# Performance work log

Measured on AMD Instinct MI355X. Metric: run time of the kernel, lower is better.

## Reference

```python
import jax, jax.numpy as jnp
import numpy as np

EMB_DIM = 768
NUM_HEADS = 12
OUT_DIM = 768


def setup_inputs() -> dict:
    key = jax.random.key(0)
    k_x, k_q, k_k, k_v, k_o = jax.random.split(key, 5)
    B, N, D = 8, 1024, EMB_DIM
    s = 1.0 / np.sqrt(D)
    return {
        "x": jax.random.normal(k_x, (B, N, D), dtype=jnp.float32),
        # torch nn.Linear weights are stored [out_features, in_features]
        "Wq": jax.random.normal(k_q, (D, D), dtype=jnp.float32) * s,
        "Wk": jax.random.normal(k_k, (D, D), dtype=jnp.float32) * s,
        "Wv": jax.random.normal(k_v, (D, D), dtype=jnp.float32) * s,
        "Wo": jax.random.normal(k_o, (OUT_DIM, D), dtype=jnp.float32) * s,
    }


def _split_heads(t, H):
    # [B, N, D] -> [B*H, N, D//H]  (heads folded into batch, per einsum 'b i d')
    B, N, D = t.shape
    return t.reshape(B, N, H, D // H).transpose(0, 2, 1, 3).reshape(B * H, N, D // H)


def _merge_heads(t, B, H):
    BH, N, dh = t.shape
    return t.reshape(B, H, N, dh).transpose(0, 2, 1, 3).reshape(B, N, H * dh)


def reference(x, Wq, Wk, Wv, Wo):
    B, N, D = x.shape
    H = NUM_HEADS
    dh = D // H
    # q/k/v projections (torch Linear: y = x @ W.T, no bias)
    q = _split_heads(x @ Wq.T, H)
    k = _split_heads(x @ Wk.T, H)
    v = _split_heads(x @ Wv.T, H)
    scale = dh ** (-0.5)
    # dots: 'b i d , b j d -> b i j' -> full [B*H, N, N] score matrix
    dots = jnp.einsum('bid,bjd->bij', q, k) * scale
    attn = jax.nn.softmax(dots, axis=-1)
    # dropout p=0.0 -> identity
    # vect: 'b i d , b d j -> b i j' == attn @ v
    vect = jnp.einsum('bij,bjd->bid', attn, v)
    out = _merge_heads(vect, B, H) @ Wo.T
    return out
```

## Files before the change

kernel.cpp:

```cpp
#include <hip/hip_runtime.h>
#include <hip/hip_bf16.h>
#include <stdint.h>


typedef __bf16 bf16x8 __attribute__((ext_vector_type(8)));
typedef __bf16 bf16x4 __attribute__((ext_vector_type(4)));
typedef float f32x4 __attribute__((ext_vector_type(4)));

#define GAS __attribute__((address_space(1)))
#define LAS __attribute__((address_space(3)))

__device__ __forceinline__ void glds16(const short* gp, short* lp) {
  __builtin_amdgcn_global_load_lds((const GAS void*)gp, (LAS void*)lp, 16, 0, 0);
}

__device__ __forceinline__ float fast_exp2(float x) {
#if __has_builtin(__builtin_amdgcn_exp2f)
  return __builtin_amdgcn_exp2f(x);
#else
  return __expf(x * 0.6931471805599453f);
#endif
}

__device__ __forceinline__ short bfbits(float f) {
  __bf16 b = (__bf16)f;
  union { __bf16 b; short s; } cv; cv.b = b;
  return cv.s;
}

__device__ __forceinline__ void stage8_f32(const float* __restrict__ src, short* dst) {
  float4 f0 = ((const float4*)src)[0];
  float4 f1 = ((const float4*)src)[1];
  bf16x8 t;
  t[0] = (__bf16)f0.x; t[1] = (__bf16)f0.y; t[2] = (__bf16)f0.z; t[3] = (__bf16)f0.w;
  t[4] = (__bf16)f1.x; t[5] = (__bf16)f1.y; t[6] = (__bf16)f1.z; t[7] = (__bf16)f1.w;
  *(bf16x8*)dst = t;
}

__global__ __launch_bounds__(256) void convert_kernel(
    const float* __restrict__ x, const float* __restrict__ Wq,
    const float* __restrict__ Wk, const float* __restrict__ Wv,
    const float* __restrict__ Wo,
    short* __restrict__ xb, short* __restrict__ wqkv, short* __restrict__ wob) {
  int u0 = blockIdx.x * 1024 + threadIdx.x;
#pragma unroll
  for (int i = 0; i < 4; ++i) {
    int u = u0 + i * 256;
    const float* src; short* dst;
    if (u < 786432) { src = x + (size_t)u * 8; dst = xb + (size_t)u * 8; }
    else if (u < 1007616) {
      int r = u - 786432;
      int wsel = r / 73728, off = r % 73728;
      const float* W = (wsel == 0) ? Wq : (wsel == 1) ? Wk : Wv;
      src = W + (size_t)off * 8;
      dst = wqkv + (size_t)r * 8;
    } else {
      int r = u - 1007616;
      src = Wo + (size_t)r * 8; dst = wob + (size_t)r * 8;
    }
    stage8_f32(src, dst);
  }
}

__device__ __forceinline__ void stage_half(const short* __restrict__ g, short* l,
                                           int w, int lane) {
#pragma unroll
  for (int p = 0; p < 2; ++p) {
    int c = (w * 2 + p) * 64 + lane;
    int row = c >> 3;
    int cs = ((c & 7) ^ (row & 7)) * 8;
    glds16(g + (size_t)row * 768 + cs, l + c * 8);
  }
}

__device__ __forceinline__ void bar_fence() {
  asm volatile("" ::: "memory");
  __builtin_amdgcn_s_barrier();
  asm volatile("" ::: "memory");
}

__device__ __forceinline__ void load_a8(const short* base, int wr, int l16, int quad,
                                        bf16x8 (&fa)[4][2]) {
#pragma unroll
  for (int mf = 0; mf < 4; ++mf)
#pragma unroll
    for (int kk = 0; kk < 2; ++kk) {
      int row = wr * 64 + mf * 16 + l16;
      fa[mf][kk] = *(const bf16x8*)&base[row * 64 + ((((kk << 2) + quad) ^ (row & 7)) << 3)];
    }
}

__device__ __forceinline__ void load_b4(const short* base, int rbase, int l16, int quad,
                                        bf16x8 (&fb)[2][2]) {
#pragma unroll
  for (int nf = 0; nf < 2; ++nf)
#pragma unroll
    for (int kk = 0; kk < 2; ++kk) {
      int row = rbase + nf * 16 + l16;
      fb[nf][kk] = *(const bf16x8*)&base[row * 64 + ((((kk << 2) + quad) ^ (row & 7)) << 3)];
    }
}

__device__ __forceinline__ void mma16(const bf16x8 (&fa)[4][2], const bf16x8 (&fb)[2][2],
                                      f32x4 (&acc)[4][4], int nf0) {
  __builtin_amdgcn_s_setprio(1);
#pragma unroll
  for (int kk = 0; kk < 2; ++kk)
#pragma unroll
    for (int mf = 0; mf < 4; ++mf)
#pragma unroll
      for (int nf = 0; nf < 2; ++nf)
        acc[mf][nf0 + nf] = __builtin_amdgcn_mfma_f32_16x16x32_bf16(
            fa[mf][kk], fb[nf][kk], acc[mf][nf0 + nf], 0, 0, 0);
  __builtin_amdgcn_s_setprio(0);
}

__global__ __launch_bounds__(512, 2) void gemm_qkv(
    const short* __restrict__ xb, const short* __restrict__ wqkv,
    short* __restrict__ q, short* __restrict__ k, short* __restrict__ vt) {
  const int lin = blockIdx.x;
  const int swz = (lin & 7) * 36 + (lin >> 3);
  const int bx = swz & 31;
  const int by = swz >> 5;
  const int m0 = bx * 256;
  const int n0g = by * 256;
  const int tid = threadIdx.x;
  const int w = tid >> 6, lane = tid & 63, l16 = lane & 15, quad = lane >> 4;
  const int wr = w >> 2, wc = w & 3;

  __shared__ short lds[2][2][2][8192];

  const short* Asrc = xb + (size_t)m0 * 768;
  const short* Bsrc = wqkv + (size_t)n0g * 768;

  f32x4 acc[2][4][4];
#pragma unroll
  for (int h = 0; h < 2; ++h)
#pragma unroll
    for (int i = 0; i < 4; ++i)
#pragma unroll
      for (int j = 0; j < 4; ++j) acc[h][i][j] = (f32x4){0.f, 0.f, 0.f, 0.f};

  stage_half(Asrc, &lds[0][0][0][0], w, lane);
  stage_half(Bsrc, &lds[0][1][0][0], w, lane);
  stage_half(Bsrc + 98304, &lds[0][1][1][0], w, lane);
  stage_half(Asrc + 98304, &lds[0][0][1][0], w, lane);
  stage_half(Asrc + 64, &lds[1][0][0][0], w, lane);
  stage_half(Bsrc + 64, &lds[1][1][0][0], w, lane);
  stage_half(Bsrc + 98304 + 64, &lds[1][1][1][0], w, lane);
  asm volatile("s_waitcnt vmcnt(6)" ::: "memory");
  bar_fence();

  const int bh = wc >> 1;
  const int rb0 = (wc & 1) * 64;
  const short* bb0 = &lds[0][1][bh][0];
  const short* bb1 = &lds[1][1][bh][0];

  bf16x8 fa[4][2], fb0[2][2], fb1[2][2];

  for (int i = 0; i < 6; ++i) {
    const int t1 = 2 * i + 1, t2 = 2 * i + 2, t3 = 2 * i + 3;
    const bool pf = (i < 5);

    load_a8(&lds[0][0][0][0], wr, l16, quad, fa);
    load_b4(bb0, rb0, l16, quad, fb0);
    stage_half(Asrc + 98304 + (size_t)t1 * 64, &lds[1][0][1][0], w, lane);
    bar_fence();
    mma16(fa, fb0, acc[0], 0);
    bar_fence();
    load_b4(bb0, rb0 + 32, l16, quad, fb1);
    if (pf) stage_half(Asrc + (size_t)t2 * 64, &lds[0][0][0][0], w, lane);
    bar_fence();
    mma16(fa, fb1, acc[0], 2);
    bar_fence();
    load_a8(&lds[0][0][1][0], wr, l16, quad, fa);
    if (pf) stage_half(Bsrc + (size_t)t2 * 64, &lds[0][1][0][0], w, lane);
    bar_fence();
    mma16(fa, fb1, acc[1], 2);
    bar_fence();
    if (pf) {
      stage_half(Bsrc + 98304 + (size_t)t2 * 64, &lds[0][1][1][0], w, lane);
      asm volatile("s_waitcnt vmcnt(6)" ::: "memory");
    } else {
      asm volatile("s_waitcnt vmcnt(0)" ::: "memory");
    }
    bar_fence();
    mma16(fa, fb0, acc[1], 0);
    bar_fence();

    load_a8(&lds[1][0][0][0], wr, l16, quad, fa);
    load_b4(bb1, rb0, l16, quad, fb0);
    if (pf) stage_half(Asrc + 98304 + (size_t)t2 * 64, &lds[0][0][1][0], w, lane);
    bar_fence();
    mma16(fa, fb0, acc[0], 0);
    bar_fence();
    load_b4(bb1, rb0 + 32, l16, quad, fb1);
    if (pf) stage_half(Asrc + (size_t)t3 * 64, &lds[1][0][0][0], w, lane);
    bar_fence();
    mma16(fa, fb1, acc[0], 2);
    bar_fence();
    load_a8(&lds[1][0][1][0], wr, l16, quad, fa);
    if (pf) stage_half(Bsrc + (size_t)t3 * 64, &lds[1][1][0][0], w, lane);
    bar_fence();
    mma16(fa, fb1, acc[1], 2);
    bar_fence();
    if (pf) stage_half(Bsrc + 98304 + (size_t)t3 * 64, &lds[1][1][1][0], w, lane);
    asm volatile("s_waitcnt vmcnt(6)" ::: "memory");
    bar_fence();
    mma16(fa, fb0, acc[1], 0);
    bar_fence();
  }

  const int wsel = by / 3;
  const int nl0 = (by % 3) * 256 + wc * 64;
  if (wsel == 2) {
#pragma unroll
    for (int h = 0; h < 2; ++h)
#pragma unroll
      for (int mf = 0; mf < 4; ++mf)
#pragma unroll
        for (int nf = 0; nf < 4; ++nf) {
          int token = m0 + h * 128 + wr * 64 + mf * 16 + quad * 4;
          int nl = nl0 + nf * 16 + l16;
          int bhh = (token >> 10) * 12 + (nl >> 6);
          short tmp[4];
#pragma unroll
          for (int r = 0; r < 4; ++r) tmp[r] = bfbits(acc[h][mf][nf][r]);
          *(uint2*)(vt + (size_t)bhh * 65536 + (size_t)(nl & 63) * 1024 + (token & 1023)) =
              *(const uint2*)tmp;
        }
  } else {
    short* C = wsel ? k : q;
    const float sc = wsel ? 1.0f : 0.1803368801111244f;
#pragma unroll
    for (int h = 0; h < 2; ++h)
#pragma unroll
      for (int mf = 0; mf < 4; ++mf)
#pragma unroll
        for (int nf = 0; nf < 4; ++nf)
#pragma unroll
          for (int r = 0; r < 4; ++r) {
            int row = m0 + h * 128 + wr * 64 + mf * 16 + quad * 4 + r;
            int nl = nl0 + nf * 16 + l16;
            C[(size_t)row * 768 + nl] = bfbits(acc[h][mf][nf][r] * sc);
          }
  }
}

__global__ __launch_bounds__(256) void attn_kernel(
    const short* __restrict__ q, const short* __restrict__ k,
    const short* __restrict__ vt, short* __restrict__ vect) {
  const int bh = blockIdx.x % 96;
  const int qt = blockIdx.x / 96;
  const int b = bh / 12, h = bh % 12;
  const int m0 = qt * 64;
  const int tid = threadIdx.x;
  const int w = tid >> 6, lane = tid & 63, l16 = lane & 15, quad = lane >> 4;

  __shared__ short sK[128 * 64];
  __shared__ short sVt[64 * 128];

  const size_t base = (size_t)b * 786432 + (size_t)h * 64;
  const size_t vbase = (size_t)bh * 65536;

#pragma unroll
  for (int p = 0; p < 2; ++p) {
    int lin = (w * 2 + p) * 64 + lane;
    int row = lin >> 3;
    int cs = ((lin & 7) ^ (row & 7)) * 8;
    glds16(q + base + (size_t)(m0 + row) * 768 + cs, &sK[lin * 8]);
  }
  __syncthreads();
  bf16x8 bq[2];
#pragma unroll
  for (int kk = 0; kk < 2; ++kk) {
    int row = w * 16 + l16;
    bq[kk] = *(const bf16x8*)&sK[row * 64 + (((kk * 4 + quad) ^ (row & 7)) << 3)];
  }

  f32x4 l4 = (f32x4){0.f, 0.f, 0.f, 0.f};
  f32x4 oacc[4];
#pragma unroll
  for (int td = 0; td < 4; ++td) oacc[td] = (f32x4){0.f, 0.f, 0.f, 0.f};

  for (int j0 = 0; j0 < 1024; j0 += 128) {
    __syncthreads();
#pragma unroll
    for (int p = 0; p < 4; ++p) {
      int lin = (w * 4 + p) * 64 + lane;
      int row = lin >> 3;
      int cs = ((lin & 7) ^ (row & 7)) * 8;
      glds16(k + base + (size_t)(j0 + row) * 768 + cs, &sK[lin * 8]);
    }
#pragma unroll
    for (int p = 0; p < 4; ++p) {
      int lin = (w * 4 + p) * 64 + lane;
      int row = lin >> 4;
      int c = lin & 15;
      int cs = (c ^ (row & 15)) * 8;
      glds16(vt + vbase + (size_t)row * 1024 + j0 + cs, &sVt[lin * 8]);
    }
    __syncthreads();

#pragma unroll
    for (int jh = 0; jh < 2; ++jh) {
      f32x4 s[4];
#pragma unroll
      for (int ti = 0; ti < 4; ++ti) s[ti] = (f32x4){0.f, 0.f, 0.f, 0.f};
#pragma unroll
      for (int kk = 0; kk < 2; ++kk)
#pragma unroll
        for (int ti = 0; ti < 4; ++ti) {
          int row = jh * 64 + ti * 16 + l16;
          bf16x8 a = *(const bf16x8*)&sK[row * 64 + (((kk * 4 + quad) ^ (row & 7)) << 3)];
          s[ti] = __builtin_amdgcn_mfma_f32_16x16x32_bf16(a, bq[kk], s[ti], 0, 0, 0);
        }

      bf16x4 pb[4];
#pragma unroll
      for (int ti = 0; ti < 4; ++ti) {
        f32x4 e;
        e[0] = fast_exp2(s[ti][0]);
        e[1] = fast_exp2(s[ti][1]);
        e[2] = fast_exp2(s[ti][2]);
        e[3] = fast_exp2(s[ti][3]);
        l4 += e;
        bf16x4 tb;
        tb[0] = (__bf16)e[0]; tb[1] = (__bf16)e[1];
        tb[2] = (__bf16)e[2]; tb[3] = (__bf16)e[3];
        pb[ti] = tb;
      }

#pragma unroll
      for (int t2 = 0; t2 < 2; ++t2) {
        union { bf16x4 hh[2]; bf16x8 v; } bp;
        bp.hh[0] = pb[2 * t2];
        bp.hh[1] = pb[2 * t2 + 1];
#pragma unroll
        for (int td = 0; td < 4; ++td) {
          int row = td * 16 + l16;
          int o1 = jh * 64 + t2 * 32 + quad * 4;
          int c1 = o1 >> 3, w1 = o1 & 7;
          int c2 = c1 + 2;
          union { uint2 u[2]; bf16x8 v; } tmp;
          tmp.u[0] = *(const uint2*)&sVt[row * 128 + ((c1 ^ (row & 15)) << 3) + w1];
          tmp.u[1] = *(const uint2*)&sVt[row * 128 + ((c2 ^ (row & 15)) << 3) + w1];
          oacc[td] = __builtin_amdgcn_mfma_f32_16x16x32_bf16(tmp.v, bp.v, oacc[td], 0, 0, 0);
        }
      }
    }
  }

  float l = (l4[0] + l4[1]) + (l4[2] + l4[3]);
  l += __shfl_xor(l, 16);
  l += __shfl_xor(l, 32);
  float inv = 1.0f / l;
  int i_tok = m0 + w * 16 + l16;
#pragma unroll
  for (int td = 0; td < 4; ++td) {
    short tmp[4];
#pragma unroll
    for (int r = 0; r < 4; ++r) tmp[r] = bfbits(oacc[td][r] * inv);
    *(uint2*)(vect + base + (size_t)i_tok * 768 + td * 16 + quad * 4) = *(const uint2*)tmp;
  }
}

__global__ __launch_bounds__(256) void gemm_out(
    const short* __restrict__ vect, const short* __restrict__ wob,
    float* __restrict__ out) {
  const int m0 = blockIdx.x * 64;
  const int n0 = blockIdx.y * 128;
  const int tid = threadIdx.x;
  const int w = tid >> 6, lane = tid & 63, l16 = lane & 15, quad = lane >> 4;
  const int wr = w >> 1, wc = w & 1;

  __shared__ short sA[64 * 64];
  __shared__ short sB[128 * 64];

  f32x4 acc[2][4];
#pragma unroll
  for (int i = 0; i < 2; ++i)
#pragma unroll
    for (int j = 0; j < 4; ++j) acc[i][j] = (f32x4){0.f, 0.f, 0.f, 0.f};

  for (int k0 = 0; k0 < 768; k0 += 64) {
    __syncthreads();
    const short* Ab = vect + (size_t)m0 * 768 + k0;
    const short* Bb = wob + (size_t)n0 * 768 + k0;
#pragma unroll
    for (int p = 0; p < 2; ++p) {
      int lin = (w * 2 + p) * 64 + lane;
      int row = lin >> 3;
      int cs = ((lin & 7) ^ (row & 7)) * 8;
      glds16(Ab + (size_t)row * 768 + cs, &sA[lin * 8]);
    }
#pragma unroll
    for (int p = 0; p < 4; ++p) {
      int lin = (w * 4 + p) * 64 + lane;
      int row = lin >> 3;
      int cs = ((lin & 7) ^ (row & 7)) * 8;
      glds16(Bb + (size_t)row * 768 + cs, &sB[lin * 8]);
    }
    __syncthreads();
#pragma unroll
    for (int kk2 = 0; kk2 < 2; ++kk2) {
      bf16x8 af[2], bfg[4];
#pragma unroll
      for (int t = 0; t < 2; ++t) {
        int ra = wr * 32 + t * 16 + l16;
        af[t] = *(const bf16x8*)&sA[ra * 64 + (((kk2 * 4 + quad) ^ (ra & 7)) << 3)];
      }
#pragma unroll
      for (int t = 0; t < 4; ++t) {
        int rb = wc * 64 + t * 16 + l16;
        bfg[t] = *(const bf16x8*)&sB[rb * 64 + (((kk2 * 4 + quad) ^ (rb & 7)) << 3)];
      }
#pragma unroll
      for (int ti = 0; ti < 2; ++ti)
#pragma unroll
        for (int tj = 0; tj < 4; ++tj)
          acc[ti][tj] = __builtin_amdgcn_mfma_f32_16x16x32_bf16(af[ti], bfg[tj], acc[ti][tj], 0, 0, 0);
    }
  }
#pragma unroll
  for (int ti = 0; ti < 2; ++ti)
#pragma unroll
    for (int tj = 0; tj < 4; ++tj)
#pragma unroll
      for (int r = 0; r < 4; ++r) {
        int row = m0 + wr * 32 + ti * 16 + quad * 4 + r;
        int col = n0 + wc * 64 + tj * 16 + l16;
        out[(size_t)row * 768 + col] = acc[ti][tj][r];
      }
}

extern "C" void kernel_launch(void* const* d_in, const int* in_sizes, int n_in,
                              void* d_out, int out_size, void* d_ws, size_t ws_size,
                              hipStream_t stream) {
  const float* x  = (const float*)d_in[0];
  const float* Wq = (const float*)d_in[1];
  const float* Wk = (const float*)d_in[2];
  const float* Wv = (const float*)d_in[3];
  const float* Wo = (const float*)d_in[4];
  float* out = (float*)d_out;

  const size_t MN = (size_t)8192 * 768;
  short* q    = (short*)d_ws;
  short* k    = q + MN;
  short* vt   = k + MN;
  short* vect = q;
  short* wob  = vt + MN;

  short* xb   = (short*)d_out;
  short* wqkv = xb + MN;

  convert_kernel<<<1056, 256, 0, stream>>>(x, Wq, Wk, Wv, Wo, xb, wqkv, wob);
  gemm_qkv<<<288, 512, 0, stream>>>(xb, wqkv, q, k, vt);
  attn_kernel<<<1536, 256, 0, stream>>>(q, k, vt, vect);
  gemm_out<<<dim3(128, 6), 256, 0, stream>>>(vect, wob, out);
}
```

Measured before the change: 200.4 us.

## Shrink QKV GEMM tile to 128x256 with triple-buffered LDS pipeline

Cuts the QKV projection block tile from 256x256 to 128x256 and doubles the grid to 576 blocks, which halves the accumulator registers and fills the CUs more evenly. The double-buffered ping-pong schedule is replaced by a three-stage LDS ring that prefetches two k-steps ahead, with sched_barriers fencing the MFMA groups. In exchange, each block reuses its loaded B tile over fewer rows, so more global and LDS traffic is spent per FLOP.

```diff
diff --git a/kernel.cpp b/kernel.cpp
--- a/kernel.cpp
+++ b/kernel.cpp
@@ -119,95 +119,70 @@
     const short* __restrict__ xb, const short* __restrict__ wqkv,
     short* __restrict__ q, short* __restrict__ k, short* __restrict__ vt) {
   const int lin = blockIdx.x;
-  const int swz = (lin & 7) * 36 + (lin >> 3);
-  const int bx = swz & 31;
-  const int by = swz >> 5;
-  const int m0 = bx * 256;
+  const int swz = (lin & 7) * 72 + (lin >> 3);
+  const int bx = swz & 63;
+  const int by = swz >> 6;
+  const int m0 = bx * 128;
   const int n0g = by * 256;
   const int tid = threadIdx.x;
   const int w = tid >> 6, lane = tid & 63, l16 = lane & 15, quad = lane >> 4;
   const int wr = w >> 2, wc = w & 3;
 
-  __shared__ short lds[2][2][2][8192];
+  __shared__ short lds[3][24576];
 
   const short* Asrc = xb + (size_t)m0 * 768;
   const short* Bsrc = wqkv + (size_t)n0g * 768;
 
-  f32x4 acc[2][4][4];
-#pragma unroll
-  for (int h = 0; h < 2; ++h)
-#pragma unroll
-    for (int i = 0; i < 4; ++i)
-#pragma unroll
-      for (int j = 0; j < 4; ++j) acc[h][i][j] = (f32x4){0.f, 0.f, 0.f, 0.f};
-
-  stage_half(Asrc, &lds[0][0][0][0], w, lane);
-  stage_half(Bsrc, &lds[0][1][0][0], w, lane);
-  stage_half(Bsrc + 98304, &lds[0][1][1][0], w, lane);
-  stage_half(Asrc + 98304, &lds[0][0][1][0], w, lane);
-  stage_half(Asrc + 64, &lds[1][0][0][0], w, lane);
-  stage_half(Bsrc + 64, &lds[1][1][0][0], w, lane);
-  stage_half(Bsrc + 98304 + 64, &lds[1][1][1][0], w, lane);
+  f32x4 acc[4][4];
+#pragma unroll
+  for (int i = 0; i < 4; ++i)
+#pragma unroll
+    for (int j = 0; j < 4; ++j) acc[i][j] = (f32x4){0.f, 0.f, 0.f, 0.f};
+
+  stage_half(Asrc, &lds[0][0], w, lane);
+  stage_half(Bsrc, &lds[0][8192], w, lane);
+  stage_half(Bsrc + 98304, &lds[0][16384], w, lane);
+  stage_half(Asrc + 64, &lds[1][0], w, lane);
+  stage_half(Bsrc + 64, &lds[1][8192], w, lane);
+  stage_half(Bsrc + 98304 + 64, &lds[1][16384], w, lane);
   asm volatile("s_waitcnt vmcnt(6)" ::: "memory");
   bar_fence();
 
   const int bh = wc >> 1;
   const int rb0 = (wc & 1) * 64;
-  const short* bb0 = &lds[0][1][bh][0];
-  const short* bb1 = &lds[1][1][bh][0];
 
   bf16x8 fa[4][2], fb0[2][2], fb1[2][2];
 
-  for (int i = 0; i < 6; ++i) {
-    const int t1 = 2 * i + 1, t2 = 2 * i + 2, t3 = 2 * i + 3;
-    const bool pf = (i < 5);
-
-    load_a8(&lds[0][0][0][0], wr, l16, quad, fa);
-    load_b4(bb0, rb0, l16, quad, fb0);
-    stage_half(Asrc + 98304 + (size_t)t1 * 64, &lds[1][0][1][0], w, lane);
+#pragma unroll
+  for (int t = 0; t < 12; ++t) {
+    const int buf = t % 3, nb = (t + 2) % 3;
+    const bool pf = (t < 10);
+    const short* A = &lds[buf][0];
+    const short* Bb = &lds[buf][8192 + bh * 8192];
+
+    load_a8(A, wr, l16, quad, fa);
+    load_b4(Bb, rb0, l16, quad, fb0);
+    if (pf) {
+      stage_half(Asrc + (size_t)(t + 2) * 64, &lds[nb][0], w, lane);
+      stage_half(Bsrc + (size_t)(t + 2) * 64, &lds[nb][8192], w, lane);
+    }
     bar_fence();
-    mma16(fa, fb0, acc[0], 0);
+    __builtin_amdgcn_sched_barrier(0);
+    mma16(fa, fb0, acc, 0);
+    __builtin_amdgcn_sched_barrier(0);
     bar_fence();
-    load_b4(bb0, rb0 + 32, l16, quad, fb1);
-    if (pf) stage_half(Asrc + (size_t)t2 * 64, &lds[0][0][0][0], w, lane);
+
+    load_b4(Bb, rb0 + 32, l16, quad, fb1);
+    if (pf) {
+      stage_half(Bsrc + 98304 + (size_t)(t + 2) * 64, &lds[nb][16384], w, lane);
+      asm volatile("s_waitcnt vmcnt(6)" ::: "memory");
+    } else if (t == 10) {
+      asm volatile("s_waitcnt vmcnt(0)" ::: "memory");
+    }
     bar_fence();
-    mma16(fa, fb1, acc[0], 2);
-    bar_fence();
-    load_a8(&lds[0][0][1][0], wr, l16, quad, fa);
-    if (pf) stage_half(Bsrc + (size_t)t2 * 64, &lds[0][1][0][0], w, lane);
-    bar_fence();
-    mma16(fa, fb1, acc[1], 2);
-    bar_fence();
-    if (pf) {
-      stage_half(Bsrc + 98304 + (size_t)t2 * 64, &lds[0][1][1][0], w, lane);
-      asm volatile("s_waitcnt vmcnt(6)" ::: "memory");
-    } else {
-      asm volatile("s_waitcnt vmcnt(0)" ::: "memory");
-    }
-    bar_fence();
-    mma16(fa, fb0, acc[1], 0);
-    bar_fence();
-
-    load_a8(&lds[1][0][0][0], wr, l16, quad, fa);
-    load_b4(bb1, rb0, l16, quad, fb0);
-    if (pf) stage_half(Asrc + 98304 + (size_t)t2 * 64, &lds[0][0][1][0], w, lane);
-    bar_fence();
-    mma16(fa, fb0, acc[0], 0);
-    bar_fence();
-    load_b4(bb1, rb0 + 32, l16, quad, fb1);
-    if (pf) stage_half(Asrc + (size_t)t3 * 64, &lds[1][0][0][0], w, lane);
-    bar_fence();
-    mma16(fa, fb1, acc[0], 2);
-    bar_fence();
-    load_a8(&lds[1][0][1][0], wr, l16, quad, fa);
-    if (pf) stage_half(Bsrc + (size_t)t3 * 64, &lds[1][1][0][0], w, lane);
-    bar_fence();
-    mma16(fa, fb1, acc[1], 2);
-    bar_fence();
-    if (pf) stage_half(Bsrc + 98304 + (size_t)t3 * 64, &lds[1][1][1][0], w, lane);
-    asm volatile("s_waitcnt vmcnt(6)" ::: "memory");
-    bar_fence();
-    mma16(fa, fb0, acc[1], 0);
+    __builtin_amdgcn_sched_barrier(0);
+    mma16(fa, fb1, acc, 2);
+    __builtin_amdgcn_sched_barrier(0);
     bar_fence();
   }
 
@@ -215,35 +190,31 @@
   const int nl0 = (by % 3) * 256 + wc * 64;
   if (wsel == 2) {
 #pragma unroll
-    for (int h = 0; h < 2; ++h)
-#pragma unroll
-      for (int mf = 0; mf < 4; ++mf)
-#pragma unroll
-        for (int nf = 0; nf < 4; ++nf) {
-          int token = m0 + h * 128 + wr * 64 + mf * 16 + quad * 4;
-          int nl = nl0 + nf * 16 + l16;
-          int bhh = (token >> 10) * 12 + (nl >> 6);
-          short tmp[4];
-#pragma unroll
-          for (int r = 0; r < 4; ++r) tmp[r] = bfbits(acc[h][mf][nf][r]);
-          *(uint2*)(vt + (size_t)bhh * 65536 + (size_t)(nl & 63) * 1024 + (token & 1023)) =
-              *(const uint2*)tmp;
-        }
+    for (int mf = 0; mf < 4; ++mf)
+#pragma unroll
+      for (int nf = 0; nf < 4; ++nf) {
+        int token = m0 + wr * 64 + mf * 16 + quad * 4;
+        int nl = nl0 + nf * 16 + l16;
+        int bhh = (token >> 10) * 12 + (nl >> 6);
+        short tmp[4];
+#pragma unroll
+        for (int r = 0; r < 4; ++r) tmp[r] = bfbits(acc[mf][nf][r]);
+        *(uint2*)(vt + (size_t)bhh * 65536 + (size_t)(nl & 63) * 1024 + (token & 1023)) =
+            *(const uint2*)tmp;
+      }
   } else {
     short* C = wsel ? k : q;
     const float sc = wsel ? 1.0f : 0.1803368801111244f;
 #pragma unroll
-    for (int h = 0; h < 2; ++h)
-#pragma unroll
-      for (int mf = 0; mf < 4; ++mf)
-#pragma unroll
-        for (int nf = 0; nf < 4; ++nf)
-#pragma unroll
-          for (int r = 0; r < 4; ++r) {
-            int row = m0 + h * 128 + wr * 64 + mf * 16 + quad * 4 + r;
-            int nl = nl0 + nf * 16 + l16;
-            C[(size_t)row * 768 + nl] = bfbits(acc[h][mf][nf][r] * sc);
-          }
+    for (int mf = 0; mf < 4; ++mf)
+#pragma unroll
+      for (int nf = 0; nf < 4; ++nf)
+#pragma unroll
+        for (int r = 0; r < 4; ++r) {
+          int row = m0 + wr * 64 + mf * 16 + quad * 4 + r;
+          int nl = nl0 + nf * 16 + l16;
+          C[(size_t)row * 768 + nl] = bfbits(acc[mf][nf][r] * sc);
+        }
   }
 }
 
@@ -455,7 +426,7 @@
   short* wqkv = xb + MN;
 
   convert_kernel<<<1056, 256, 0, stream>>>(x, Wq, Wk, Wv, Wo, xb, wqkv, wob);
-  gemm_qkv<<<288, 512, 0, stream>>>(xb, wqkv, q, k, vt);
+  gemm_qkv<<<576, 512, 0, stream>>>(xb, wqkv, q, k, vt);
   attn_kernel<<<1536, 256, 0, stream>>>(q, k, vt, vect);
   gemm_out<<<dim3(128, 6), 256, 0, stream>>>(vect, wob, out);
 }
```

After: 194.1 us. -3.2%, faster.
